# Kernel optimization log

Hardware: AMD Instinct MI355X
Metric: run time of the kernel (lower is better)

Reference implementation:

```python
import jax, jax.numpy as jnp
import numpy as np

H = 12          # num_attention_heads
DH = 64         # attention_head_size (768/12)
LDH = 16        # layout head size (DH / channel_shrink_ratio=4)


def _split_heads(x, h, d):
    # [B,S,h*d] -> [B,h,S,d]
    B, S, _ = x.shape
    return x.reshape(B, S, h, d).transpose(0, 2, 1, 3)


def setup_inputs() -> dict:
    key = jax.random.key(0)
    ks = jax.random.split(key, 16)
    B, S, D, LD = 4, 2048, 768, 192
    std = 0.02
    inp = {
        "hidden_states": jax.random.normal(ks[0], (B, S, D), jnp.float32),
        "layout_hidden_states": jax.random.normal(ks[1], (B, S, LD), jnp.float32),
        "attention_mask": jnp.zeros((B, 1, 1, S), jnp.float32),
        # text-stream QKV (weights stored [in, out] so y = x @ W + b)
        "Wq": jax.random.normal(ks[2], (D, D), jnp.float32) * std,
        "bq": jnp.zeros((D,), jnp.float32),
        "Wk": jax.random.normal(ks[3], (D, D), jnp.float32) * std,
        "bk": jnp.zeros((D,), jnp.float32),
        "Wv": jax.random.normal(ks[4], (D, D), jnp.float32) * std,
        "bv": jnp.zeros((D,), jnp.float32),
        # layout-stream QKV
        "LWq": jax.random.normal(ks[5], (LD, LD), jnp.float32) * std,
        "Lbq": jnp.zeros((LD,), jnp.float32),
        "LWk": jax.random.normal(ks[6], (LD, LD), jnp.float32) * std,
        "Lbk": jnp.zeros((LD,), jnp.float32),
        "LWv": jax.random.normal(ks[7], (LD, LD), jnp.float32) * std,
        "Lbv": jnp.zeros((LD,), jnp.float32),
    }
    return inp


def reference(hidden_states, layout_hidden_states, attention_mask,
              Wq, bq, Wk, bk, Wv, bv, LWq, Lbq, LWk, Lbk, LWv, Lbv):
    B, S, D = hidden_states.shape
    LD = layout_hidden_states.shape[-1]

    q = _split_heads(hidden_states @ Wq + bq, H, DH)   # [B,H,S,DH]
    k = _split_heads(hidden_states @ Wk + bk, H, DH)
    v = _split_heads(hidden_states @ Wv + bv, H, DH)
    lq = _split_heads(layout_hidden_states @ LWq + Lbq, H, LDH)  # [B,H,S,LDH]
    lk = _split_heads(layout_hidden_states @ LWk + Lbk, H, LDH)
    lv = _split_heads(layout_hidden_states @ LWv + Lbv, H, LDH)

    # scaled per-stream scores
    scores_t = jnp.einsum('bhqd,bhkd->bhqk', q, k) / np.sqrt(DH).astype(np.float32)
    scores_l = jnp.einsum('bhqd,bhkd->bhqk', lq, lk) / np.sqrt(LDH).astype(np.float32)

    # bidirectional cross-addition (BiACM); layout branch detaches the text scores
    scores_text = scores_t + scores_l + attention_mask
    scores_layout = jax.lax.stop_gradient(scores_t) + scores_l + attention_mask

    probs_t = jax.nn.softmax(scores_text, axis=-1)
    probs_l = jax.nn.softmax(scores_layout, axis=-1)

    ctx = jnp.einsum('bhqk,bhkd->bhqd', probs_t, v)
    ctx = ctx.transpose(0, 2, 1, 3).reshape(B, S, H * DH)       # [B,S,768]
    lctx = jnp.einsum('bhqk,bhkd->bhqd', probs_l, lv)
    lctx = lctx.transpose(0, 2, 1, 3).reshape(B, S, H * LDH)    # [B,S,192]
    return (ctx, lctx)
```

## Files before the change

kernel.cpp:

```cpp
#include <hip/hip_runtime.h>
#include <hip/hip_bf16.h>
#include <cstdint>
#include <math.h>

typedef __attribute__((ext_vector_type(8))) short bf16x8;
typedef __attribute__((ext_vector_type(4))) short bf16x4;
typedef __attribute__((ext_vector_type(4))) float f32x4;
typedef __attribute__((ext_vector_type(16))) float f32x16;

#define MFMA16(a, b, c) __builtin_amdgcn_mfma_f32_16x16x32_bf16((a), (b), (c), 0, 0, 0)
#define MFMA32(a, b, c) __builtin_amdgcn_mfma_f32_32x32x16_bf16((a), (b), (c), 0, 0, 0)

static __device__ __forceinline__ unsigned short f2b(float x) {
  __hip_bfloat16 h = __float2bfloat16(x);
  return __builtin_bit_cast(unsigned short, h);
}

static __device__ __forceinline__ void gload16(const void* g, void* l) {
  __builtin_amdgcn_global_load_lds((const __attribute__((address_space(1))) void*)g,
                                   (__attribute__((address_space(3))) void*)l, 16, 0, 0);
}

#define INVLN2 1.4426950408889634f

__global__ __launch_bounds__(256) void cvt_f32_bf16(const float* __restrict__ s,
                                                    __hip_bfloat16* __restrict__ d, int n) {
  int stride = gridDim.x * 256 * 4;
  for (int i = (blockIdx.x * 256 + threadIdx.x) * 4; i < n; i += stride) {
    float4 v = *(const float4*)(s + i);
    ushort4 o;
    o.x = f2b(v.x); o.y = f2b(v.y); o.z = f2b(v.z); o.w = f2b(v.w);
    *(ushort4*)&d[i] = o;
  }
}

__global__ __launch_bounds__(256) void transpose_cvt(const float* __restrict__ s0,
                                                     const float* __restrict__ s1,
                                                     const float* __restrict__ s2,
                                                     __hip_bfloat16* __restrict__ dst,
                                                     int K, int N, int Npad) {
  __shared__ float tile[32][33];
  int p = blockIdx.z;
  const float* src = (p == 0) ? s0 : (p == 1) ? s1 : s2;
  int n0 = blockIdx.x * 32, k0 = blockIdx.y * 32;
  int tx = threadIdx.x & 31, ty = threadIdx.x >> 5;
  for (int i = ty; i < 32; i += 8) {
    int k = k0 + i, n = n0 + tx;
    tile[i][tx] = (k < K && n < N) ? src[(size_t)k * N + n] : 0.f;
  }
  __syncthreads();
  for (int i = ty; i < 32; i += 8) {
    int n = n0 + i, k = k0 + tx;
    if (n < Npad && k < K)
      dst[(size_t)p * Npad * K + (size_t)n * K + k] = __float2bfloat16(tile[tx][i]);
  }
}

template <int K, int N, int NPAD, int HD, int COFF>
__global__ __launch_bounds__(256, 2) void proj_gemm(
    const __hip_bfloat16* __restrict__ X, const __hip_bfloat16* __restrict__ Wt,
    const float* __restrict__ bq, const float* __restrict__ bk, const float* __restrict__ bv,
    __hip_bfloat16* __restrict__ qc, __hip_bfloat16* __restrict__ kc,
    __hip_bfloat16* __restrict__ vt, float qscale) {
  __shared__ __hip_bfloat16 lA[128 * 32];
  __shared__ __hip_bfloat16 lB[128 * 32];
  const int tid = threadIdx.x, w = tid >> 6, l = tid & 63;
  const int lr = l & 15, lg = l >> 4;
  const int p = blockIdx.z;
  const int m0 = blockIdx.x * 128, n0 = blockIdx.y * 128;
  const __hip_bfloat16* Wp = Wt + (size_t)p * NPAD * K;
  const float* bias = (p == 0) ? bq : (p == 1) ? bk : bv;
  const float scale = (p == 0) ? qscale : 1.0f;

  f32x4 acc[4][4] = {};

  const int srow = (w * 2) * 16 + (l >> 2);
  const int scol = (l & 3) * 8;
  const __hip_bfloat16* gA = X + (size_t)(m0 + srow) * K + scol;
  const __hip_bfloat16* gB = Wp + (size_t)(n0 + srow) * K + scol;
  __hip_bfloat16* dA = lA + (w * 2) * 512;
  __hip_bfloat16* dB = lB + (w * 2) * 512;
  const int wr = w >> 1, wc = w & 1;

  for (int kk = 0; kk < K; kk += 32) {
    gload16(gA + kk, dA);
    gload16(gA + (size_t)16 * K + kk, dA + 512);
    gload16(gB + kk, dB);
    gload16(gB + (size_t)16 * K + kk, dB + 512);
    __syncthreads();
    bf16x8 af[4], bfr[4];
#pragma unroll
    for (int i = 0; i < 4; i++) af[i] = *(const bf16x8*)(lA + (wr * 64 + i * 16 + lr) * 32 + lg * 8);
#pragma unroll
    for (int j = 0; j < 4; j++) bfr[j] = *(const bf16x8*)(lB + (wc * 64 + j * 16 + lr) * 32 + lg * 8);
#pragma unroll
    for (int i = 0; i < 4; i++)
#pragma unroll
      for (int j = 0; j < 4; j++) acc[i][j] = MFMA16(bfr[j], af[i], acc[i][j]);
    __syncthreads();
  }

#pragma unroll
  for (int j = 0; j < 4; j++) {
    int nb = n0 + wc * 64 + j * 16 + lg * 4;
    if (NPAD > N && nb >= N) continue;
    float4 bv4 = *(const float4*)(bias + nb);
    int hh = nb / HD, d0 = nb % HD;
#pragma unroll
    for (int i = 0; i < 4; i++) {
      int m = m0 + wr * 64 + i * 16 + lr;
      int bb = m >> 11, s = m & 2047;
      if (p == 2) {
        size_t based = ((size_t)(bb * 12 + hh) * 80 + COFF + d0) * 2048 + s;
        vt[based]          = __float2bfloat16(acc[i][j][0] + bv4.x);
        vt[based + 2048]   = __float2bfloat16(acc[i][j][1] + bv4.y);
        vt[based + 4096]   = __float2bfloat16(acc[i][j][2] + bv4.z);
        vt[based + 6144]   = __float2bfloat16(acc[i][j][3] + bv4.w);
      } else {
        size_t base = ((size_t)(bb * 12 + hh) * 2048 + s) * 80 + COFF + d0;
        ushort4 st;
        st.x = f2b((acc[i][j][0] + bv4.x) * scale);
        st.y = f2b((acc[i][j][1] + bv4.y) * scale);
        st.z = f2b((acc[i][j][2] + bv4.z) * scale);
        st.w = f2b((acc[i][j][3] + bv4.w) * scale);
        *(ushort4*)((p == 0 ? qc : kc) + base) = st;
      }
    }
  }
}

__global__ __launch_bounds__(256, 3) void attn_kernel(
    const __hip_bfloat16* __restrict__ qc, const __hip_bfloat16* __restrict__ kc,
    const __hip_bfloat16* __restrict__ vt, const float* __restrict__ mask,
    float* __restrict__ out, float* __restrict__ out2) {
  __shared__ __hip_bfloat16 lK[2][10 * 512];
  __shared__ __hip_bfloat16 lV[2][8 * 776];
  const int tid = threadIdx.x, w = tid >> 6, l = tid & 63;
  const int hi = l >> 5, ln = l & 31;
  const int bh = blockIdx.y, b_ = bh / 12, h = bh - b_ * 12;
  const int q0 = blockIdx.x * 128;

  const __hip_bfloat16* kbase = kc + ((size_t)bh * 2048 + l) * 80;
  const __hip_bfloat16* vbase = vt + (size_t)bh * 80 * 2048;
  const float* maskb = mask + b_ * 2048;

  const int vd0 = tid >> 3, va0 = tid & 7;
  const int vd1 = (tid + 256) >> 3, va1 = tid & 7;
  const int vd2 = (tid + 512) >> 3, va2 = tid & 7;

  bf16x8 aq[5];
  {
    const __hip_bfloat16* qp = qc + ((size_t)bh * 2048 + q0 + w * 32 + ln) * 80 + hi * 8;
#pragma unroll
    for (int t = 0; t < 5; ++t) aq[t] = *(const bf16x8*)(qp + t * 16);
  }

  {
    int buf = tid >> 7, g = (tid >> 4) & 7, row = 80 + (tid & 15);
    short v = (row == 80) ? (short)0x3F80 : (short)0;
    bf16x8 x = {v, v, v, v, v, v, v, v};
    *(bf16x8*)(&lV[buf][g * 776 + row * 8]) = x;
  }
  {
    const __hip_bfloat16* kg = kbase;
    gload16(kg + w * 8, &lK[0][w * 512]);
    gload16(kg + (4 + w) * 8, &lK[0][(4 + w) * 512]);
    if (w < 2) gload16(kg + (8 + w) * 8, &lK[0][(8 + w) * 512]);
    bf16x8 v0 = *(const bf16x8*)(vbase + (size_t)vd0 * 2048 + va0 * 8);
    bf16x8 v1 = *(const bf16x8*)(vbase + (size_t)vd1 * 2048 + va1 * 8);
    *(bf16x4*)(&lV[0][(va0 & 6) * 776 + vd0 * 8 + (va0 & 1) * 4]) = bf16x4{v0[0], v0[1], v0[2], v0[3]};
    *(bf16x4*)(&lV[0][((va0 & 6) | 1) * 776 + vd0 * 8 + (va0 & 1) * 4]) = bf16x4{v0[4], v0[5], v0[6], v0[7]};
    *(bf16x4*)(&lV[0][(va1 & 6) * 776 + vd1 * 8 + (va1 & 1) * 4]) = bf16x4{v1[0], v1[1], v1[2], v1[3]};
    *(bf16x4*)(&lV[0][((va1 & 6) | 1) * 776 + vd1 * 8 + (va1 & 1) * 4]) = bf16x4{v1[4], v1[5], v1[6], v1[7]};
    if (tid < 128) {
      bf16x8 v2 = *(const bf16x8*)(vbase + (size_t)vd2 * 2048 + va2 * 8);
      *(bf16x4*)(&lV[0][(va2 & 6) * 776 + vd2 * 8 + (va2 & 1) * 4]) = bf16x4{v2[0], v2[1], v2[2], v2[3]};
      *(bf16x4*)(&lV[0][((va2 & 6) | 1) * 776 + vd2 * 8 + (va2 & 1) * 4]) = bf16x4{v2[4], v2[5], v2[6], v2[7]};
    }
  }
  __syncthreads();

  float mrun = -INFINITY;
  f32x16 o0 = {}, o1 = {}, o2 = {};

  for (int kt = 0; kt < 32; ++kt) {
    const int cur = kt & 1, nxt = cur ^ 1;
    const int kvn = (kt + 1 < 32) ? (kt + 1) * 64 : kt * 64;
    const int kv0 = kt * 64;

    {
      const __hip_bfloat16* kg = kbase + (size_t)kvn * 80;
      gload16(kg + w * 8, &lK[nxt][w * 512]);
      gload16(kg + (4 + w) * 8, &lK[nxt][(4 + w) * 512]);
      if (w < 2) gload16(kg + (8 + w) * 8, &lK[nxt][(8 + w) * 512]);
    }
    bf16x8 v0 = *(const bf16x8*)(vbase + (size_t)vd0 * 2048 + kvn + va0 * 8);
    bf16x8 v1 = *(const bf16x8*)(vbase + (size_t)vd1 * 2048 + kvn + va1 * 8);
    bf16x8 v2;
    if (tid < 128) v2 = *(const bf16x8*)(vbase + (size_t)vd2 * 2048 + kvn + va2 * 8);

    const __hip_bfloat16* lKc = &lK[cur][0];
    f32x16 sf0 = {}, sf1 = {};
#pragma unroll
    for (int t = 0; t < 5; ++t) {
      bf16x8 ak0 = *(const bf16x8*)(lKc + (t * 2 + hi) * 512 + ln * 8);
      bf16x8 ak1 = *(const bf16x8*)(lKc + (t * 2 + hi) * 512 + (32 + ln) * 8);
      sf0 = MFMA32(ak0, aq[t], sf0);
      sf1 = MFMA32(ak1, aq[t], sf1);
    }

    float s_[2][16];
#pragma unroll
    for (int q = 0; q < 4; ++q) {
      float4 m0 = *(const float4*)(maskb + kv0 + 4 * hi + q * 8);
      float4 m1 = *(const float4*)(maskb + kv0 + 32 + 4 * hi + q * 8);
#pragma unroll
      for (int c = 0; c < 4; ++c) {
        s_[0][q * 4 + c] = sf0[q * 4 + c] + ((const float*)&m0)[c] * INVLN2;
        s_[1][q * 4 + c] = sf1[q * 4 + c] + ((const float*)&m1)[c] * INVLN2;
      }
    }

    float tm = s_[0][0];
#pragma unroll
    for (int r = 1; r < 16; ++r) tm = fmaxf(tm, s_[0][r]);
#pragma unroll
    for (int r = 0; r < 16; ++r) tm = fmaxf(tm, s_[1][r]);
    tm = fmaxf(tm, __shfl_xor(tm, 32));
    if (__any(tm > mrun + 8.f)) {
      float nm = fmaxf(mrun, tm);
      float alpha = exp2f(mrun - nm);
      mrun = nm;
#pragma unroll
      for (int r = 0; r < 16; ++r) {
        float a = __shfl(alpha, (r & 3) + 8 * (r >> 2) + 4 * hi);
        o0[r] *= a; o1[r] *= a; o2[r] *= a;
      }
    }

    bf16x8 pa[2][2];
#pragma unroll
    for (int kb = 0; kb < 2; ++kb)
#pragma unroll
      for (int ks = 0; ks < 2; ++ks) {
        bf16x8 pk;
#pragma unroll
        for (int j = 0; j < 8; ++j)
          pk[j] = (short)f2b(exp2f(s_[kb][ks * 8 + j] - mrun));
        pa[kb][ks] = pk;
      }

    const __hip_bfloat16* lVc = &lV[cur][0];
#pragma unroll
    for (int kb = 0; kb < 2; ++kb)
#pragma unroll
      for (int ks = 0; ks < 2; ++ks) {
        const int g = (kb * 2 + ks) * 2 + hi;
        bf16x8 bv0 = *(const bf16x8*)(lVc + g * 776 + ln * 8);
        bf16x8 bv1 = *(const bf16x8*)(lVc + g * 776 + (32 + ln) * 8);
        bf16x8 bv2 = *(const bf16x8*)(lVc + g * 776 + (64 + ln) * 8);
        o0 = MFMA32(pa[kb][ks], bv0, o0);
        o1 = MFMA32(pa[kb][ks], bv1, o1);
        o2 = MFMA32(pa[kb][ks], bv2, o2);
      }

    *(bf16x4*)(&lV[nxt][(va0 & 6) * 776 + vd0 * 8 + (va0 & 1) * 4]) = bf16x4{v0[0], v0[1], v0[2], v0[3]};
    *(bf16x4*)(&lV[nxt][((va0 & 6) | 1) * 776 + vd0 * 8 + (va0 & 1) * 4]) = bf16x4{v0[4], v0[5], v0[6], v0[7]};
    *(bf16x4*)(&lV[nxt][(va1 & 6) * 776 + vd1 * 8 + (va1 & 1) * 4]) = bf16x4{v1[0], v1[1], v1[2], v1[3]};
    *(bf16x4*)(&lV[nxt][((va1 & 6) | 1) * 776 + vd1 * 8 + (va1 & 1) * 4]) = bf16x4{v1[4], v1[5], v1[6], v1[7]};
    if (tid < 128) {
      *(bf16x4*)(&lV[nxt][(va2 & 6) * 776 + vd2 * 8 + (va2 & 1) * 4]) = bf16x4{v2[0], v2[1], v2[2], v2[3]};
      *(bf16x4*)(&lV[nxt][((va2 & 6) | 1) * 776 + vd2 * 8 + (va2 & 1) * 4]) = bf16x4{v2[4], v2[5], v2[6], v2[7]};
    }
    __syncthreads();
  }

#pragma unroll
  for (int r = 0; r < 16; ++r) {
    float den = __shfl(o2[r], 16 | (l & 32));
    float inv = 1.0f / den;
    int qg = q0 + w * 32 + (r & 3) + 8 * (r >> 2) + 4 * hi;
    size_t rowb = (size_t)b_ * 2048 + qg;
    out[rowb * 768 + h * 64 + ln] = o0[r] * inv;
    out[rowb * 768 + h * 64 + 32 + ln] = o1[r] * inv;
    if (ln < 16) out2[rowb * 192 + h * 16 + ln] = o2[r] * inv;
  }
}

extern "C" void kernel_launch(void* const* d_in, const int* in_sizes, int n_in,
                              void* d_out, int out_size, void* d_ws, size_t ws_size,
                              hipStream_t stream) {
  const float* hidden = (const float*)d_in[0];
  const float* lhidden = (const float*)d_in[1];
  const float* mask = (const float*)d_in[2];
  const float* Wq = (const float*)d_in[3];
  const float* bq = (const float*)d_in[4];
  const float* Wk = (const float*)d_in[5];
  const float* bk = (const float*)d_in[6];
  const float* Wv = (const float*)d_in[7];
  const float* bv = (const float*)d_in[8];
  const float* LWq = (const float*)d_in[9];
  const float* Lbq = (const float*)d_in[10];
  const float* LWk = (const float*)d_in[11];
  const float* Lbk = (const float*)d_in[12];
  const float* LWv = (const float*)d_in[13];
  const float* Lbv = (const float*)d_in[14];

  char* ws = (char*)d_ws;
  __hip_bfloat16* Xb  = (__hip_bfloat16*)(ws + 0);
  __hip_bfloat16* LXb = (__hip_bfloat16*)(ws + 12582912);
  __hip_bfloat16* Wt  = (__hip_bfloat16*)(ws + 15728640);
  __hip_bfloat16* LWt = (__hip_bfloat16*)(ws + 19267584);
  __hip_bfloat16* qcb = (__hip_bfloat16*)(ws + 19562496);
  __hip_bfloat16* kcb = (__hip_bfloat16*)(ws + 35291136);
  __hip_bfloat16* vtb = (__hip_bfloat16*)(ws + 51019776);

  float* out = (float*)d_out;
  float* out2 = out + (size_t)4 * 2048 * 768;

  cvt_f32_bf16<<<2048, 256, 0, stream>>>(hidden, Xb, 6291456);
  cvt_f32_bf16<<<1024, 256, 0, stream>>>(lhidden, LXb, 1572864);
  transpose_cvt<<<dim3(24, 24, 3), 256, 0, stream>>>(Wq, Wk, Wv, Wt, 768, 768, 768);
  transpose_cvt<<<dim3(8, 6, 3), 256, 0, stream>>>(LWq, LWk, LWv, LWt, 192, 192, 256);

  proj_gemm<768, 768, 768, 64, 0><<<dim3(64, 6, 3), 256, 0, stream>>>(
      Xb, Wt, bq, bk, bv, qcb, kcb, vtb, 0.125f * INVLN2);
  proj_gemm<192, 192, 256, 16, 64><<<dim3(64, 2, 3), 256, 0, stream>>>(
      LXb, LWt, Lbq, Lbk, Lbv, qcb, kcb, vtb, 0.25f * INVLN2);

  attn_kernel<<<dim3(16, 48), 256, 0, stream>>>(qcb, kcb, vtb, mask, out, out2);
}
```

Baseline: 291.6 us.

## Double-buffer projection GEMM loads and fold pre-scaled mask into score accumulator

```diff
diff --git a/kernel.cpp b/kernel.cpp
--- a/kernel.cpp
+++ b/kernel.cpp
@@ -31,6 +31,16 @@
     ushort4 o;
     o.x = f2b(v.x); o.y = f2b(v.y); o.z = f2b(v.z); o.w = f2b(v.w);
     *(ushort4*)&d[i] = o;
+  }
+}
+
+__global__ __launch_bounds__(256) void maskx_scale(const float* __restrict__ s,
+                                                   float* __restrict__ d, int n) {
+  int i = (blockIdx.x * 256 + threadIdx.x) * 4;
+  if (i < n) {
+    float4 v = *(const float4*)(s + i);
+    v.x *= INVLN2; v.y *= INVLN2; v.z *= INVLN2; v.w *= INVLN2;
+    *(float4*)(d + i) = v;
   }
 }
 
@@ -62,8 +72,8 @@
     const float* __restrict__ bq, const float* __restrict__ bk, const float* __restrict__ bv,
     __hip_bfloat16* __restrict__ qc, __hip_bfloat16* __restrict__ kc,
     __hip_bfloat16* __restrict__ vt, float qscale) {
-  __shared__ __hip_bfloat16 lA[128 * 32];
-  __shared__ __hip_bfloat16 lB[128 * 32];
+  __shared__ __hip_bfloat16 lA[2][128 * 32];
+  __shared__ __hip_bfloat16 lB[2][128 * 32];
   const int tid = threadIdx.x, w = tid >> 6, l = tid & 63;
   const int lr = l & 15, lg = l >> 4;
   const int p = blockIdx.z;
@@ -78,26 +88,34 @@
   const int scol = (l & 3) * 8;
   const __hip_bfloat16* gA = X + (size_t)(m0 + srow) * K + scol;
   const __hip_bfloat16* gB = Wp + (size_t)(n0 + srow) * K + scol;
-  __hip_bfloat16* dA = lA + (w * 2) * 512;
-  __hip_bfloat16* dB = lB + (w * 2) * 512;
+  const int wo = (w * 2) * 512;
   const int wr = w >> 1, wc = w & 1;
-
-  for (int kk = 0; kk < K; kk += 32) {
-    gload16(gA + kk, dA);
-    gload16(gA + (size_t)16 * K + kk, dA + 512);
-    gload16(gB + kk, dB);
-    gload16(gB + (size_t)16 * K + kk, dB + 512);
+  constexpr int NK = K / 32;
+
+  gload16(gA, &lA[0][wo]);
+  gload16(gA + (size_t)16 * K, &lA[0][wo + 512]);
+  gload16(gB, &lB[0][wo]);
+  gload16(gB + (size_t)16 * K, &lB[0][wo + 512]);
+
+  for (int t = 0; t < NK; ++t) {
+    const int cur = t & 1;
     __syncthreads();
+    if (t + 1 < NK) {
+      const int nx = cur ^ 1, kk = (t + 1) * 32;
+      gload16(gA + kk, &lA[nx][wo]);
+      gload16(gA + (size_t)16 * K + kk, &lA[nx][wo + 512]);
+      gload16(gB + kk, &lB[nx][wo]);
+      gload16(gB + (size_t)16 * K + kk, &lB[nx][wo + 512]);
+    }
     bf16x8 af[4], bfr[4];
 #pragma unroll
-    for (int i = 0; i < 4; i++) af[i] = *(const bf16x8*)(lA + (wr * 64 + i * 16 + lr) * 32 + lg * 8);
-#pragma unroll
-    for (int j = 0; j < 4; j++) bfr[j] = *(const bf16x8*)(lB + (wc * 64 + j * 16 + lr) * 32 + lg * 8);
+    for (int i = 0; i < 4; i++) af[i] = *(const bf16x8*)(&lA[cur][(wr * 64 + i * 16 + lr) * 32 + lg * 8]);
+#pragma unroll
+    for (int j = 0; j < 4; j++) bfr[j] = *(const bf16x8*)(&lB[cur][(wc * 64 + j * 16 + lr) * 32 + lg * 8]);
 #pragma unroll
     for (int i = 0; i < 4; i++)
 #pragma unroll
       for (int j = 0; j < 4; j++) acc[i][j] = MFMA16(bfr[j], af[i], acc[i][j]);
-    __syncthreads();
   }
 
 #pragma unroll
@@ -131,7 +149,7 @@
 
 __global__ __launch_bounds__(256, 3) void attn_kernel(
     const __hip_bfloat16* __restrict__ qc, const __hip_bfloat16* __restrict__ kc,
-    const __hip_bfloat16* __restrict__ vt, const float* __restrict__ mask,
+    const __hip_bfloat16* __restrict__ vt, const float* __restrict__ mxb,
     float* __restrict__ out, float* __restrict__ out2) {
   __shared__ __hip_bfloat16 lK[2][10 * 512];
   __shared__ __hip_bfloat16 lV[2][8 * 776];
@@ -142,7 +160,7 @@
 
   const __hip_bfloat16* kbase = kc + ((size_t)bh * 2048 + l) * 80;
   const __hip_bfloat16* vbase = vt + (size_t)bh * 80 * 2048;
-  const float* maskb = mask + b_ * 2048;
+  const float* maskb = mxb + b_ * 2048;
 
   const int vd0 = tid >> 3, va0 = tid & 7;
   const int vd1 = (tid + 256) >> 3, va1 = tid & 7;
@@ -199,8 +217,15 @@
     bf16x8 v2;
     if (tid < 128) v2 = *(const bf16x8*)(vbase + (size_t)vd2 * 2048 + kvn + va2 * 8);
 
+    f32x16 sf0, sf1;
+#pragma unroll
+    for (int q = 0; q < 4; ++q) {
+      float4 m0 = *(const float4*)(maskb + kv0 + 4 * hi + q * 8);
+      float4 m1 = *(const float4*)(maskb + kv0 + 32 + 4 * hi + q * 8);
+      sf0[q * 4 + 0] = m0.x; sf0[q * 4 + 1] = m0.y; sf0[q * 4 + 2] = m0.z; sf0[q * 4 + 3] = m0.w;
+      sf1[q * 4 + 0] = m1.x; sf1[q * 4 + 1] = m1.y; sf1[q * 4 + 2] = m1.z; sf1[q * 4 + 3] = m1.w;
+    }
     const __hip_bfloat16* lKc = &lK[cur][0];
-    f32x16 sf0 = {}, sf1 = {};
 #pragma unroll
     for (int t = 0; t < 5; ++t) {
       bf16x8 ak0 = *(const bf16x8*)(lKc + (t * 2 + hi) * 512 + ln * 8);
@@ -209,23 +234,11 @@
       sf1 = MFMA32(ak1, aq[t], sf1);
     }
 
-    float s_[2][16];
-#pragma unroll
-    for (int q = 0; q < 4; ++q) {
-      float4 m0 = *(const float4*)(maskb + kv0 + 4 * hi + q * 8);
-      float4 m1 = *(const float4*)(maskb + kv0 + 32 + 4 * hi + q * 8);
-#pragma unroll
-      for (int c = 0; c < 4; ++c) {
-        s_[0][q * 4 + c] = sf0[q * 4 + c] + ((const float*)&m0)[c] * INVLN2;
-        s_[1][q * 4 + c] = sf1[q * 4 + c] + ((const float*)&m1)[c] * INVLN2;
-      }
-    }
-
-    float tm = s_[0][0];
-#pragma unroll
-    for (int r = 1; r < 16; ++r) tm = fmaxf(tm, s_[0][r]);
-#pragma unroll
-    for (int r = 0; r < 16; ++r) tm = fmaxf(tm, s_[1][r]);
+    float tm = fmaxf(sf0[0], sf0[1]);
+#pragma unroll
+    for (int r = 2; r < 16; r += 2) tm = fmaxf(fmaxf(tm, sf0[r]), sf0[r + 1]);
+#pragma unroll
+    for (int r = 0; r < 16; r += 2) tm = fmaxf(fmaxf(tm, sf1[r]), sf1[r + 1]);
     tm = fmaxf(tm, __shfl_xor(tm, 32));
     if (__any(tm > mrun + 8.f)) {
       float nm = fmaxf(mrun, tm);
@@ -240,15 +253,16 @@
 
     bf16x8 pa[2][2];
 #pragma unroll
-    for (int kb = 0; kb < 2; ++kb)
-#pragma unroll
-      for (int ks = 0; ks < 2; ++ks) {
-        bf16x8 pk;
-#pragma unroll
-        for (int j = 0; j < 8; ++j)
-          pk[j] = (short)f2b(exp2f(s_[kb][ks * 8 + j] - mrun));
-        pa[kb][ks] = pk;
+    for (int ks = 0; ks < 2; ++ks) {
+      bf16x8 pk0, pk1;
+#pragma unroll
+      for (int j = 0; j < 8; ++j) {
+        pk0[j] = (short)f2b(exp2f(sf0[ks * 8 + j] - mrun));
+        pk1[j] = (short)f2b(exp2f(sf1[ks * 8 + j] - mrun));
       }
+      pa[0][ks] = pk0;
+      pa[1][ks] = pk1;
+    }
 
     const __hip_bfloat16* lVc = &lV[cur][0];
 #pragma unroll
@@ -314,12 +328,14 @@
   __hip_bfloat16* qcb = (__hip_bfloat16*)(ws + 19562496);
   __hip_bfloat16* kcb = (__hip_bfloat16*)(ws + 35291136);
   __hip_bfloat16* vtb = (__hip_bfloat16*)(ws + 51019776);
+  float*          mxb = (float*)(ws + 66748416);
 
   float* out = (float*)d_out;
   float* out2 = out + (size_t)4 * 2048 * 768;
 
   cvt_f32_bf16<<<2048, 256, 0, stream>>>(hidden, Xb, 6291456);
   cvt_f32_bf16<<<1024, 256, 0, stream>>>(lhidden, LXb, 1572864);
+  maskx_scale<<<8, 256, 0, stream>>>(mask, mxb, 8192);
   transpose_cvt<<<dim3(24, 24, 3), 256, 0, stream>>>(Wq, Wk, Wv, Wt, 768, 768, 768);
   transpose_cvt<<<dim3(8, 6, 3), 256, 0, stream>>>(LWq, LWk, LWv, LWt, 192, 192, 256);
 
@@ -328,5 +344,5 @@
   proj_gemm<192, 192, 256, 16, 64><<<dim3(64, 2, 3), 256, 0, stream>>>(
       LXb, LWt, Lbq, Lbk, Lbv, qcb, kcb, vtb, 0.25f * INVLN2);
 
-  attn_kernel<<<dim3(16, 48), 256, 0, stream>>>(qcb, kcb, vtb, mask, out, out2);
-}
+  attn_kernel<<<dim3(16, 48), 256, 0, stream>>>(qcb, kcb, vtb, mxb, out, out2);
+}
```

Measured after the change: 287.5 us. About the same (-1.4%).
